# Kernel tuning notes

Measured on AMD Instinct MI355X. Metric: run time of the kernel, lower is better.

The kernel has to match this reference:

```python
import jax, jax.numpy as jnp
import numpy as np

N = 50000
E = 1600000
IN_FEATS = 256
HIDDEN = 32
HEADS = 4
NUM_CLASSES = 16
NEG_SLOPE = 0.2  # DGL GATConv default leaky_relu slope


def gat_conv(x, src, dst, W, b, attn_l, attn_r, n_nodes):
    """DGL-style GATConv. x:[N,Fin], W:[Fin,H*D], attn_l/attn_r:[H,D], b:[H*D].
    Returns [N, H, D]."""
    H, D = attn_l.shape
    feat = (x @ W).reshape(-1, H, D)                     # [N,H,D]
    el = jnp.sum(feat * attn_l, axis=-1)                 # [N,H]
    er = jnp.sum(feat * attn_r, axis=-1)                 # [N,H]
    e = jax.nn.leaky_relu(el[src] + er[dst], NEG_SLOPE)  # [E,H]
    # segment softmax over incoming edges of each dst node
    m = jax.ops.segment_max(e, dst, num_segments=n_nodes)
    m = jnp.where(jnp.isfinite(m), m, 0.0)               # empty segments -> -inf
    ex = jnp.exp(e - m[dst])                             # [E,H]
    denom = jax.ops.segment_sum(ex, dst, num_segments=n_nodes)
    alpha = ex / jnp.maximum(denom, 1e-9)[dst]           # [E,H]
    msg = feat[src] * alpha[:, :, None]                  # [E,H,D]
    out = jax.ops.segment_sum(msg, dst, num_segments=n_nodes)
    return out + b.reshape(H, D)


def setup_inputs() -> dict:
    key = jax.random.key(0)
    ks = jax.random.split(key, 12)
    x = jax.random.normal(ks[0], (N, IN_FEATS), dtype=jnp.float32)
    src = jax.random.randint(ks[1], (E,), 0, N, dtype=jnp.int32)
    dst = jax.random.randint(ks[2], (E,), 0, N, dtype=jnp.int32)
    s1 = 1.0 / np.sqrt(IN_FEATS)
    W1 = jax.random.normal(ks[3], (IN_FEATS, HEADS * HIDDEN), dtype=jnp.float32) * s1
    b1 = jnp.zeros((HEADS * HIDDEN,), dtype=jnp.float32)
    al1 = jax.random.normal(ks[4], (HEADS, HIDDEN), dtype=jnp.float32) * 0.1
    ar1 = jax.random.normal(ks[5], (HEADS, HIDDEN), dtype=jnp.float32) * 0.1
    F2 = HEADS * HIDDEN
    s2 = 1.0 / np.sqrt(F2)
    W2 = jax.random.normal(ks[6], (F2, NUM_CLASSES), dtype=jnp.float32) * s2
    b2 = jnp.zeros((NUM_CLASSES,), dtype=jnp.float32)
    al2 = jax.random.normal(ks[7], (1, NUM_CLASSES), dtype=jnp.float32) * 0.1
    ar2 = jax.random.normal(ks[8], (1, NUM_CLASSES), dtype=jnp.float32) * 0.1
    return {"x": x, "src": src, "dst": dst,
            "W1": W1, "b1": b1, "al1": al1, "ar1": ar1,
            "W2": W2, "b2": b2, "al2": al2, "ar2": ar2}


def reference(x, src, dst, W1, b1, al1, ar1, W2, b2, al2, ar2):
    h = jax.nn.elu(gat_conv(x, src, dst, W1, b1, al1, ar1, N))  # [N,H,D]
    h = h.reshape(N, HEADS * HIDDEN)                            # flatten(1)
    out = gat_conv(h, src, dst, W2, b2, al2, ar2, N)            # [N,1,C]
    return out.mean(axis=1)                                     # [N,C]
```

## Files before the change

### kernel.cpp

```cpp
#include <hip/hip_runtime.h>
#include <hip/hip_fp16.h>

#define N_NODES 50000
#define N_EDGES 1600000
#define FIN 256
#define HD 128
#define NHEADS 4
#define C2 16
#define NEG 0.2f

#define EBLK 4096
#define NBLK 391
#define NBUCK 391
#define BSH 7
#define BMASK 127
#define MAXB 5120

typedef _Float16 v8h __attribute__((ext_vector_type(8)));
typedef float v4f __attribute__((ext_vector_type(4)));
union F4H8 { float4 f; v8h h; };

__device__ __forceinline__ float elu1(float x) { return x > 0.f ? x : __expf(x) - 1.f; }
__device__ __forceinline__ float lexp(float e) { return __expf(e > 0.f ? e : NEG * e); }


__global__ __launch_bounds__(256) void k_bhist(const int* __restrict__ dst,
                                               int* __restrict__ ghist) {
    __shared__ int lh[NBUCK];
    int tid = threadIdx.x, b = blockIdx.x;
    for (int t = tid; t < NBUCK; t += 256) lh[t] = 0;
    __syncthreads();
    int base = b * EBLK;
    int nq = (min(EBLK, N_EDGES - base)) >> 2;
    const int4* d4 = (const int4*)(dst + base);
    for (int q = tid; q < nq; q += 256) {
        int4 d = d4[q];
        atomicAdd(&lh[d.x >> BSH], 1);
        atomicAdd(&lh[d.y >> BSH], 1);
        atomicAdd(&lh[d.z >> BSH], 1);
        atomicAdd(&lh[d.w >> BSH], 1);
    }
    __syncthreads();
    for (int t = tid; t < NBUCK; t += 256) ghist[t * NBLK + b] = lh[t];
}

__global__ __launch_bounds__(256) void k_bscan1(int* __restrict__ ghist,
                                                int* __restrict__ bucket_tot) {
    __shared__ int s[256];
    int B = blockIdx.x, t = threadIdx.x;
    int* row = ghist + (size_t)B * NBLK;
    int i0 = 2 * t, i1 = 2 * t + 1;
    int a0 = (i0 < NBLK) ? row[i0] : 0;
    int a1 = (i1 < NBLK) ? row[i1] : 0;
    int pair = a0 + a1;
    s[t] = pair;
    __syncthreads();
    for (int off = 1; off < 256; off <<= 1) {
        int u = (t >= off) ? s[t - off] : 0;
        __syncthreads();
        s[t] += u;
        __syncthreads();
    }
    int excl = s[t] - pair;
    if (i0 < NBLK) row[i0] = excl;
    if (i1 < NBLK) row[i1] = excl + a0;
    if (t == 255) bucket_tot[B] = s[255];
}

__global__ __launch_bounds__(512) void k_bscan2(const int* __restrict__ bucket_tot,
                                                int* __restrict__ bucket_base,
                                                int* __restrict__ rowstart) {
    __shared__ int s[512];
    int t = threadIdx.x;
    int v = (t < NBUCK) ? bucket_tot[t] : 0;
    s[t] = v;
    __syncthreads();
    for (int off = 1; off < 512; off <<= 1) {
        int u = (t >= off) ? s[t - off] : 0;
        __syncthreads();
        s[t] += u;
        __syncthreads();
    }
    if (t < NBUCK) bucket_base[t] = s[t] - v;
    if (t == 0) { bucket_base[NBUCK] = N_EDGES; rowstart[N_NODES] = N_EDGES; }
}

__global__ __launch_bounds__(256) void k_bscatter(
        const int* __restrict__ src, const int* __restrict__ dst,
        const int* __restrict__ ghist, const int* __restrict__ bucket_base,
        int* __restrict__ ebuf) {
    __shared__ int lcur[NBUCK];
    int tid = threadIdx.x, b = blockIdx.x;
    for (int t = tid; t < NBUCK; t += 256)
        lcur[t] = bucket_base[t] + ghist[t * NBLK + b];
    __syncthreads();
    int base = b * EBLK;
    int nq = (min(EBLK, N_EDGES - base)) >> 2;
    const int4* s4 = (const int4*)(src + base);
    const int4* d4 = (const int4*)(dst + base);
    for (int q = tid; q < nq; q += 256) {
        int4 s = s4[q];
        int4 d = d4[q];
        int p;
        p = atomicAdd(&lcur[d.x >> BSH], 1); ebuf[p] = (s.x << BSH) | (d.x & BMASK);
        p = atomicAdd(&lcur[d.y >> BSH], 1); ebuf[p] = (s.y << BSH) | (d.y & BMASK);
        p = atomicAdd(&lcur[d.z >> BSH], 1); ebuf[p] = (s.z << BSH) | (d.z & BMASK);
        p = atomicAdd(&lcur[d.w >> BSH], 1); ebuf[p] = (s.w << BSH) | (d.w & BMASK);
    }
}

__global__ __launch_bounds__(256) void k_bsort(
        const int* __restrict__ ebuf, const int* __restrict__ bucket_base,
        int* __restrict__ sorted_src, int* __restrict__ rowstart) {
    __shared__ int ein[MAXB];
    __shared__ int eout[MAXB];
    __shared__ int hist[128];
    __shared__ int sc[128];
    __shared__ int cursor[128];
    int tid = threadIdx.x, B = blockIdx.x;
    int base = bucket_base[B];
    int n = bucket_base[B + 1] - base;
    if (tid < 128) hist[tid] = 0;
    __syncthreads();
    for (int i = tid; i < n; i += 256) {
        int v = ebuf[base + i];
        ein[i] = v;
        atomicAdd(&hist[v & BMASK], 1);
    }
    __syncthreads();
    if (tid < 128) sc[tid] = hist[tid];
    __syncthreads();
    for (int off = 1; off < 128; off <<= 1) {
        int u = 0;
        if (tid < 128 && tid >= off) u = sc[tid - off];
        __syncthreads();
        if (tid < 128) sc[tid] += u;
        __syncthreads();
    }
    if (tid < 128) {
        int ex = sc[tid] - hist[tid];
        cursor[tid] = ex;
        int node = B * 128 + tid;
        if (node < N_NODES) rowstart[node] = base + ex;
    }
    __syncthreads();
    for (int i = tid; i < n; i += 256) {
        int v = ein[i];
        int p = atomicAdd(&cursor[v & BMASK], 1);
        eout[p] = v >> BSH;
    }
    __syncthreads();
    for (int i = tid; i < n; i += 256) sorted_src[base + i] = eout[i];
}


__global__ __launch_bounds__(256) void k_w1half(const float* __restrict__ W1,
                                                _Float16* __restrict__ W1T) {
    int idx = blockIdx.x * 256 + threadIdx.x;
    int k = idx >> 7, c = idx & 127;
    W1T[c * 256 + k] = (_Float16)W1[idx];
}


__global__ __launch_bounds__(256) void k_gemm1(
        const float* __restrict__ x, const _Float16* __restrict__ W1T,
        const float* __restrict__ al1, const float* __restrict__ ar1,
        __half* __restrict__ feat1h, float* __restrict__ el1, float* __restrict__ er1) {
    __shared__ v8h As[64 * 4];
    __shared__ v8h Bs[128 * 4];
    int tid = threadIdx.x;
    int nb = blockIdx.x * 64;
    int wid = tid >> 6, lane = tid & 63;
    int wm = wid & 1, wn = wid >> 1;
    int q = lane >> 4, lm = lane & 15;

    int anode = tid >> 2, ach = tid & 3;
    int gnode = nb + anode; if (gnode >= N_NODES) gnode = N_NODES - 1;
    const float4* xrow = (const float4*)(x + (size_t)gnode * FIN);
    int bc = tid >> 2, bch = tid & 3;

    v4f acc[2][4];
    #pragma unroll
    for (int mt = 0; mt < 2; mt++)
        #pragma unroll
        for (int nt = 0; nt < 4; nt++) acc[mt][nt] = (v4f)(0.f);

    float4 xa0 = xrow[ach * 2];
    float4 xa1 = xrow[ach * 2 + 1];
    F4H8 wb0, wb1;
    wb0.f = *(const float4*)(W1T + bc * 256 + bch * 8);
    wb1.f = *(const float4*)(W1T + (bc + 64) * 256 + bch * 8);

    for (int step = 0; step < 8; step++) {
        __syncthreads();
        {
            v8h av;
            av[0] = (_Float16)xa0.x; av[1] = (_Float16)xa0.y;
            av[2] = (_Float16)xa0.z; av[3] = (_Float16)xa0.w;
            av[4] = (_Float16)xa1.x; av[5] = (_Float16)xa1.y;
            av[6] = (_Float16)xa1.z; av[7] = (_Float16)xa1.w;
            As[anode * 4 + (ach ^ (anode & 3))] = av;
            Bs[bc * 4 + (bch ^ (bc & 3))] = wb0.h;
            Bs[(bc + 64) * 4 + (bch ^ (bc & 3))] = wb1.h;
        }
        __syncthreads();
        if (step < 7) {
            int k0 = (step + 1) * 32;
            xa0 = xrow[(k0 >> 2) + ach * 2];
            xa1 = xrow[(k0 >> 2) + ach * 2 + 1];
            wb0.f = *(const float4*)(W1T + bc * 256 + k0 + bch * 8);
            wb1.f = *(const float4*)(W1T + (bc + 64) * 256 + k0 + bch * 8);
        }
        v8h af[2], bf[4];
        #pragma unroll
        for (int mt = 0; mt < 2; mt++) {
            int nl = wm * 32 + mt * 16 + lm;
            af[mt] = As[nl * 4 + (q ^ (nl & 3))];
        }
        #pragma unroll
        for (int nt = 0; nt < 4; nt++) {
            int cl = wn * 64 + nt * 16 + lm;
            bf[nt] = Bs[cl * 4 + (q ^ (cl & 3))];
        }
        #pragma unroll
        for (int mt = 0; mt < 2; mt++)
            #pragma unroll
            for (int nt = 0; nt < 4; nt++)
                acc[mt][nt] = __builtin_amdgcn_mfma_f32_16x16x32_f16(
                    af[mt], bf[nt], acc[mt][nt], 0, 0, 0);
    }

    float alv[4], arv[4];
    #pragma unroll
    for (int nt = 0; nt < 4; nt++) {
        alv[nt] = al1[wn * 64 + nt * 16 + lm];
        arv[nt] = ar1[wn * 64 + nt * 16 + lm];
    }
    int h0 = 2 * wn, h1 = 2 * wn + 1;
    #pragma unroll
    for (int mt = 0; mt < 2; mt++) {
        #pragma unroll
        for (int r = 0; r < 4; r++) {
            int node = nb + wm * 32 + mt * 16 + q * 4 + r;
            bool ok = node < N_NODES;
            float v0 = acc[mt][0][r], v1 = acc[mt][1][r];
            float v2 = acc[mt][2][r], v3 = acc[mt][3][r];
            if (ok) {
                __half* fp = feat1h + (size_t)node * HD + wn * 64 + lm;
                fp[0]  = __float2half(v0);
                fp[16] = __float2half(v1);
                fp[32] = __float2half(v2);
                fp[48] = __float2half(v3);
            }
            float pl0 = v0 * alv[0] + v1 * alv[1];
            float pr0 = v0 * arv[0] + v1 * arv[1];
            float pl1 = v2 * alv[2] + v3 * alv[3];
            float pr1 = v2 * arv[2] + v3 * arv[3];
            #pragma unroll
            for (int m = 1; m <= 8; m <<= 1) {
                pl0 += __shfl_xor(pl0, m); pr0 += __shfl_xor(pr0, m);
                pl1 += __shfl_xor(pl1, m); pr1 += __shfl_xor(pr1, m);
            }
            if (ok && lm == 0) {
                el1[node * 4 + h0] = pl0; er1[node * 4 + h0] = pr0;
                el1[node * 4 + h1] = pl1; er1[node * 4 + h1] = pr1;
            }
        }
    }
}


__global__ __launch_bounds__(256) void k_agg1(
        const int* __restrict__ rowstart, const int* __restrict__ sorted_src,
        const float* __restrict__ el1, const float* __restrict__ er1,
        const __half* __restrict__ feat1h, const float* __restrict__ b1,
        float* __restrict__ h) {
    int tid = threadIdx.x;
    int d = blockIdx.x * 4 + (tid >> 6);
    int lane = tid & 63;
    int eg = lane >> 4;
    int cl = lane & 15;
    int head = cl >> 2;
    float er = er1[d * 4 + head];
    int start = rowstart[d], end = rowstart[d + 1];
    float acc[8];
    #pragma unroll
    for (int k = 0; k < 8; k++) acc[k] = 0.f;
    float wsum = 0.f;

    for (int i = start; i < end; i += 16) {
        int s[4]; bool ok[4];
        #pragma unroll
        for (int u = 0; u < 4; u++) {
            int e = i + 4 * u + eg;
            ok[u] = e < end;
            int ec = ok[u] ? e : end - 1;
            s[u] = sorted_src[ec];
        }
        float elv[4];
        #pragma unroll
        for (int u = 0; u < 4; u++) elv[u] = el1[s[u] * 4 + head];
        float4 r[4];
        #pragma unroll
        for (int u = 0; u < 4; u++)
            r[u] = *(const float4*)(feat1h + (size_t)s[u] * HD + cl * 8);
        #pragma unroll
        for (int u = 0; u < 4; u++) {
            float w = ok[u] ? lexp(elv[u] + er) : 0.f;
            const __half2* p = (const __half2*)&r[u];
            #pragma unroll
            for (int q = 0; q < 4; q++) {
                float2 f = __half22float2(p[q]);
                acc[2 * q]     += w * f.x;
                acc[2 * q + 1] += w * f.y;
            }
            wsum += w;
        }
    }
    #pragma unroll
    for (int k = 0; k < 8; k++) {
        acc[k] += __shfl_xor(acc[k], 16);
        acc[k] += __shfl_xor(acc[k], 32);
    }
    wsum += __shfl_xor(wsum, 16);
    wsum += __shfl_xor(wsum, 32);
    if (eg == 0) {
        float inv = 1.f / fmaxf(wsum, 1e-9f);
        float v[8];
        #pragma unroll
        for (int k = 0; k < 8; k++) v[k] = elu1(acc[k] * inv + b1[cl * 8 + k]);
        float4* hp = (float4*)(h + (size_t)d * HD + cl * 8);
        hp[0] = make_float4(v[0], v[1], v[2], v[3]);
        hp[1] = make_float4(v[4], v[5], v[6], v[7]);
    }
}


__global__ __launch_bounds__(256) void k_gemm2(
        const float* __restrict__ h, const float* __restrict__ W2,
        const float* __restrict__ al2, const float* __restrict__ ar2,
        float* __restrict__ feat2, float* __restrict__ el2, float* __restrict__ er2) {
    __shared__ float hs[16 * 132];
    __shared__ float w2t[16 * 132];
    int tid = threadIdx.x;
    int nb = blockIdx.x * 16;
    for (int idx = tid; idx < 512; idx += 256) {
        int row = idx >> 5, kk = idx & 31;
        ((float4*)(hs + row * 132))[kk] = ((const float4*)h)[(size_t)(nb + row) * 32 + kk];
    }
    for (int idx = tid; idx < 2048; idx += 256) {
        int k = idx >> 4, c = idx & 15;
        w2t[c * 132 + k] = W2[idx];
    }
    __syncthreads();
    int nl = tid >> 4, col = tid & 15;
    const float4* hv = (const float4*)(hs + nl * 132);
    const float4* wv = (const float4*)(w2t + col * 132);
    float acc = 0.f;
    #pragma unroll
    for (int kk = 0; kk < 32; kk++) {
        float4 a = hv[kk], w = wv[kk];
        acc += a.x * w.x + a.y * w.y + a.z * w.z + a.w * w.w;
    }
    int node = nb + nl;
    feat2[node * 16 + col] = acc;
    float pl = acc * al2[col], pr = acc * ar2[col];
    #pragma unroll
    for (int m = 8; m >= 1; m >>= 1) {
        pl += __shfl_xor(pl, m);
        pr += __shfl_xor(pr, m);
    }
    if (col == 0) { el2[node] = pl; er2[node] = pr; }
}


__global__ __launch_bounds__(256) void k_agg2(
        const int* __restrict__ rowstart, const int* __restrict__ sorted_src,
        const float* __restrict__ el2, const float* __restrict__ er2,
        const float* __restrict__ feat2, const float* __restrict__ b2,
        float* __restrict__ out) {
    int tid = threadIdx.x;
    int d = blockIdx.x * 4 + (tid >> 6);
    int lane = tid & 63;
    int eg = lane >> 2;
    int cq = lane & 3;
    float er = er2[d];
    int start = rowstart[d], end = rowstart[d + 1];
    float4 acc = make_float4(0.f, 0.f, 0.f, 0.f);
    float wsum = 0.f;
    for (int i = start; i < end; i += 16) {
        int e = i + eg;
        bool ok = e < end;
        int ec = ok ? e : end - 1;
        int s = sorted_src[ec];
        float elv = el2[s];
        float4 f = ((const float4*)feat2)[(size_t)s * 4 + cq];
        float ev = elv + er;
        float wr = __expf(ev > 0.f ? ev : NEG * ev);
        float w = ok ? wr : 0.f;
        acc.x += w * f.x; acc.y += w * f.y; acc.z += w * f.z; acc.w += w * f.w;
        wsum += w;
    }
    #pragma unroll
    for (int m = 4; m <= 32; m <<= 1) {
        acc.x += __shfl_xor(acc.x, m);
        acc.y += __shfl_xor(acc.y, m);
        acc.z += __shfl_xor(acc.z, m);
        acc.w += __shfl_xor(acc.w, m);
        wsum  += __shfl_xor(wsum, m);
    }
    if (lane < 4) {
        float inv = 1.f / fmaxf(wsum, 1e-9f);
        float4 bv = ((const float4*)b2)[cq];
        float4 o = make_float4(acc.x * inv + bv.x, acc.y * inv + bv.y,
                               acc.z * inv + bv.z, acc.w * inv + bv.w);
        ((float4*)out)[(size_t)d * 4 + cq] = o;
    }
}


extern "C" void kernel_launch(void* const* d_in, const int* in_sizes, int n_in,
                              void* d_out, int out_size, void* d_ws, size_t ws_size,
                              hipStream_t stream) {
    const float* x   = (const float*)d_in[0];
    const int*   src = (const int*)d_in[1];
    const int*   dst = (const int*)d_in[2];
    const float* W1  = (const float*)d_in[3];
    const float* b1  = (const float*)d_in[4];
    const float* al1 = (const float*)d_in[5];
    const float* ar1 = (const float*)d_in[6];
    const float* W2  = (const float*)d_in[7];
    const float* b2  = (const float*)d_in[8];
    const float* al2 = (const float*)d_in[9];
    const float* ar2 = (const float*)d_in[10];
    float* out = (float*)d_out;

    char* ws = (char*)d_ws;
    size_t off = 0;
    auto alloc = [&](size_t bytes) -> char* {
        char* p = ws + off;
        off += (bytes + 255) & ~(size_t)255;
        return p;
    };
    __half* feat1h     = (__half*)alloc((size_t)N_NODES * HD * 2);
    _Float16* W1T      = (_Float16*)alloc((size_t)FIN * HD * 2);
    float* h           = (float*)alloc((size_t)N_NODES * HD * 4);
    float* el1         = (float*)alloc((size_t)N_NODES * 4 * 4);
    float* er1         = (float*)alloc((size_t)N_NODES * 4 * 4);
    float* feat2       = (float*)alloc((size_t)N_NODES * C2 * 4);
    float* el2         = (float*)alloc((size_t)N_NODES * 4);
    float* er2         = (float*)alloc((size_t)N_NODES * 4);
    int*   ghist       = (int*)alloc((size_t)NBUCK * NBLK * 4);
    int*   bucket_tot  = (int*)alloc((size_t)NBUCK * 4);
    int*   bucket_base = (int*)alloc((size_t)(NBUCK + 1) * 4);
    int*   rowstart    = (int*)alloc((size_t)(N_NODES + 1) * 4);
    int*   ebuf        = (int*)alloc((size_t)N_EDGES * 4);
    int*   sorted_src  = (int*)alloc((size_t)N_EDGES * 4);

    k_bhist<<<NBLK, 256, 0, stream>>>(dst, ghist);
    k_bscan1<<<NBUCK, 256, 0, stream>>>(ghist, bucket_tot);
    k_bscan2<<<1, 512, 0, stream>>>(bucket_tot, bucket_base, rowstart);
    k_bscatter<<<NBLK, 256, 0, stream>>>(src, dst, ghist, bucket_base, ebuf);
    k_bsort<<<NBUCK, 256, 0, stream>>>(ebuf, bucket_base, sorted_src, rowstart);
    k_w1half<<<128, 256, 0, stream>>>(W1, W1T);
    k_gemm1<<<(N_NODES + 63) / 64, 256, 0, stream>>>(x, W1T, al1, ar1, feat1h, el1, er1);
    k_agg1<<<N_NODES / 4, 256, 0, stream>>>(rowstart, sorted_src, el1, er1, feat1h, b1, h);
    k_gemm2<<<N_NODES / 16, 256, 0, stream>>>(h, W2, al2, ar2, feat2, el2, er2);
    k_agg2<<<N_NODES / 4, 256, 0, stream>>>(rowstart, sorted_src, el2, er2, feat2, b2, out);
}
```

Baseline: 244.2 us.

## Store layer-1 features head-major and aggregate one head per wavefront

Result: slower. 289.3 us (+18.5%).

```diff
diff --git a/kernel.cpp b/kernel.cpp
--- a/kernel.cpp
+++ b/kernel.cpp
@@ -165,7 +165,7 @@
 __global__ __launch_bounds__(256) void k_gemm1(
         const float* __restrict__ x, const _Float16* __restrict__ W1T,
         const float* __restrict__ al1, const float* __restrict__ ar1,
-        __half* __restrict__ feat1h, float* __restrict__ el1, float* __restrict__ er1) {
+        __half* __restrict__ feath, float* __restrict__ el1, float* __restrict__ er1) {
     __shared__ v8h As[64 * 4];
     __shared__ v8h Bs[128 * 4];
     int tid = threadIdx.x;
@@ -246,11 +246,12 @@
             float v0 = acc[mt][0][r], v1 = acc[mt][1][r];
             float v2 = acc[mt][2][r], v3 = acc[mt][3][r];
             if (ok) {
-                __half* fp = feat1h + (size_t)node * HD + wn * 64 + lm;
-                fp[0]  = __float2half(v0);
-                fp[16] = __float2half(v1);
-                fp[32] = __float2half(v2);
-                fp[48] = __float2half(v3);
+                __half* fp0 = feath + ((size_t)h0 * N_NODES + node) * 32 + lm;
+                __half* fp1 = feath + ((size_t)h1 * N_NODES + node) * 32 + lm;
+                fp0[0]  = __float2half(v0);
+                fp0[16] = __float2half(v1);
+                fp1[0]  = __float2half(v2);
+                fp1[16] = __float2half(v3);
             }
             float pl0 = v0 * alv[0] + v1 * alv[1];
             float pr0 = v0 * arv[0] + v1 * arv[1];
@@ -273,44 +274,44 @@
 __global__ __launch_bounds__(256) void k_agg1(
         const int* __restrict__ rowstart, const int* __restrict__ sorted_src,
         const float* __restrict__ el1, const float* __restrict__ er1,
-        const __half* __restrict__ feat1h, const float* __restrict__ b1,
+        const __half* __restrict__ feath, const float* __restrict__ b1,
         float* __restrict__ h) {
-    int tid = threadIdx.x;
-    int d = blockIdx.x * 4 + (tid >> 6);
-    int lane = tid & 63;
-    int eg = lane >> 4;
-    int cl = lane & 15;
-    int head = cl >> 2;
+    int p = blockIdx.x * 4 + (threadIdx.x >> 6);
+    int head = p / N_NODES;
+    int d = p - head * N_NODES;
+    int lane = threadIdx.x & 63;
+    int eg = lane >> 2;
+    int cq = lane & 3;
     float er = er1[d * 4 + head];
     int start = rowstart[d], end = rowstart[d + 1];
+    const float4* fb = (const float4*)feath + (size_t)head * N_NODES * 4;
     float acc[8];
     #pragma unroll
     for (int k = 0; k < 8; k++) acc[k] = 0.f;
     float wsum = 0.f;
 
-    for (int i = start; i < end; i += 16) {
-        int s[4]; bool ok[4];
-        #pragma unroll
-        for (int u = 0; u < 4; u++) {
-            int e = i + 4 * u + eg;
+    for (int i = start; i < end; i += 32) {
+        int s[2]; bool ok[2];
+        #pragma unroll
+        for (int u = 0; u < 2; u++) {
+            int e = i + 16 * u + eg;
             ok[u] = e < end;
             int ec = ok[u] ? e : end - 1;
             s[u] = sorted_src[ec];
         }
-        float elv[4];
-        #pragma unroll
-        for (int u = 0; u < 4; u++) elv[u] = el1[s[u] * 4 + head];
-        float4 r[4];
-        #pragma unroll
-        for (int u = 0; u < 4; u++)
-            r[u] = *(const float4*)(feat1h + (size_t)s[u] * HD + cl * 8);
-        #pragma unroll
-        for (int u = 0; u < 4; u++) {
+        float elv[2];
+        #pragma unroll
+        for (int u = 0; u < 2; u++) elv[u] = el1[s[u] * 4 + head];
+        float4 r[2];
+        #pragma unroll
+        for (int u = 0; u < 2; u++) r[u] = fb[(size_t)s[u] * 4 + cq];
+        #pragma unroll
+        for (int u = 0; u < 2; u++) {
             float w = ok[u] ? lexp(elv[u] + er) : 0.f;
-            const __half2* p = (const __half2*)&r[u];
+            const __half2* ph = (const __half2*)&r[u];
             #pragma unroll
             for (int q = 0; q < 4; q++) {
-                float2 f = __half22float2(p[q]);
+                float2 f = __half22float2(ph[q]);
                 acc[2 * q]     += w * f.x;
                 acc[2 * q + 1] += w * f.y;
             }
@@ -319,17 +320,22 @@
     }
     #pragma unroll
     for (int k = 0; k < 8; k++) {
+        acc[k] += __shfl_xor(acc[k], 4);
+        acc[k] += __shfl_xor(acc[k], 8);
         acc[k] += __shfl_xor(acc[k], 16);
         acc[k] += __shfl_xor(acc[k], 32);
     }
+    wsum += __shfl_xor(wsum, 4);
+    wsum += __shfl_xor(wsum, 8);
     wsum += __shfl_xor(wsum, 16);
     wsum += __shfl_xor(wsum, 32);
     if (eg == 0) {
         float inv = 1.f / fmaxf(wsum, 1e-9f);
         float v[8];
         #pragma unroll
-        for (int k = 0; k < 8; k++) v[k] = elu1(acc[k] * inv + b1[cl * 8 + k]);
-        float4* hp = (float4*)(h + (size_t)d * HD + cl * 8);
+        for (int k = 0; k < 8; k++)
+            v[k] = elu1(acc[k] * inv + b1[head * 32 + cq * 8 + k]);
+        float4* hp = (float4*)(h + (size_t)d * HD + head * 32 + cq * 8);
         hp[0] = make_float4(v[0], v[1], v[2], v[3]);
         hp[1] = make_float4(v[4], v[5], v[6], v[7]);
     }
@@ -442,7 +448,7 @@
         off += (bytes + 255) & ~(size_t)255;
         return p;
     };
-    __half* feat1h     = (__half*)alloc((size_t)N_NODES * HD * 2);
+    __half* feath      = (__half*)alloc((size_t)N_NODES * HD * 2);
     _Float16* W1T      = (_Float16*)alloc((size_t)FIN * HD * 2);
     float* h           = (float*)alloc((size_t)N_NODES * HD * 4);
     float* el1         = (float*)alloc((size_t)N_NODES * 4 * 4);
@@ -463,8 +469,8 @@
     k_bscatter<<<NBLK, 256, 0, stream>>>(src, dst, ghist, bucket_base, ebuf);
     k_bsort<<<NBUCK, 256, 0, stream>>>(ebuf, bucket_base, sorted_src, rowstart);
     k_w1half<<<128, 256, 0, stream>>>(W1, W1T);
-    k_gemm1<<<(N_NODES + 63) / 64, 256, 0, stream>>>(x, W1T, al1, ar1, feat1h, el1, er1);
-    k_agg1<<<N_NODES / 4, 256, 0, stream>>>(rowstart, sorted_src, el1, er1, feat1h, b1, h);
+    k_gemm1<<<(N_NODES + 63) / 64, 256, 0, stream>>>(x, W1T, al1, ar1, feath, el1, er1);
+    k_agg1<<<(N_NODES * NHEADS) / 4, 256, 0, stream>>>(rowstart, sorted_src, el1, er1, feath, b1, h);
     k_gemm2<<<N_NODES / 16, 256, 0, stream>>>(h, W2, al2, ar2, feat2, el2, er2);
     k_agg2<<<N_NODES / 4, 256, 0, stream>>>(rowstart, sorted_src, el2, er2, feat2, b2, out);
 }
```
